# Performance work log

Measured on AMD Instinct MI355X. Metric: run time of the kernel, lower is better.

Reference implementation:

```python
import jax, jax.numpy as jnp
import numpy as np

B, L, C, H = 8, 2048, 256, 4
D = C // H  # head_dim = 64
EPS = 1e-5


def setup_inputs() -> dict:
    key = jax.random.key(0)
    ks = jax.random.split(key, 16)
    s = lambda fan_in: 1.0 / np.sqrt(fan_in)
    inp = {
        'x0': jax.random.normal(ks[0], (B, L, C), jnp.float32),
        'x1': jax.random.normal(ks[1], (B, L, C), jnp.float32),
        # attention projections (stored as (in, out); torch Linear is x @ W.T + b)
        'Wqk': jax.random.normal(ks[2], (C, C), jnp.float32) * s(C),
        'bqk': jax.random.normal(ks[3], (C,), jnp.float32) * s(C),
        'Wv': jax.random.normal(ks[4], (C, C), jnp.float32) * s(C),
        'bv': jax.random.normal(ks[5], (C,), jnp.float32) * s(C),
        'Wout': jax.random.normal(ks[6], (C, C), jnp.float32) * s(C),
        'bout': jax.random.normal(ks[7], (C,), jnp.float32) * s(C),
        # shared FFN: Linear(2C->2C) -> LayerNorm -> GELU -> Linear(2C->C)
        'W1': jax.random.normal(ks[8], (2 * C, 2 * C), jnp.float32) * s(2 * C),
        'b1': jax.random.normal(ks[9], (2 * C,), jnp.float32) * s(2 * C),
        'ln_g': jnp.ones((2 * C,), jnp.float32),
        'ln_b': jnp.zeros((2 * C,), jnp.float32),
        'W2': jax.random.normal(ks[10], (2 * C, C), jnp.float32) * s(2 * C),
        'b2': jax.random.normal(ks[11], (C,), jnp.float32) * s(2 * C),
    }
    return inp


def _heads(t):
    # (B, L, C) -> (B, H, L, D)
    b, l, _ = t.shape
    return t.reshape(b, l, H, D).transpose(0, 2, 1, 3)


def _merge(t):
    # (B, H, L, D) -> (B, L, C)
    b, h, l, d = t.shape
    return t.transpose(0, 2, 1, 3).reshape(b, l, h * d)


def _ffn(z, W1, b1, ln_g, ln_b, W2, b2):
    h = z @ W1 + b1
    mu = jnp.mean(h, axis=-1, keepdims=True)
    var = jnp.var(h, axis=-1, keepdims=True)
    h = (h - mu) * jax.lax.rsqrt(var + EPS) * ln_g + ln_b
    h = jax.nn.gelu(h, approximate=False)
    return h @ W2 + b2


def reference(x0, x1, Wqk, bqk, Wv, bv, Wout, bout, W1, b1, ln_g, ln_b, W2, b2):
    scale_sqrt = D ** (-0.25)  # sqrt(head_dim**-0.5), applied to both sides
    qk0 = _heads(x0 @ Wqk + bqk) * scale_sqrt  # (B,H,M,D)
    qk1 = _heads(x1 @ Wqk + bqk) * scale_sqrt  # (B,H,N,D)
    v0 = _heads(x0 @ Wv + bv)
    v1 = _heads(x1 @ Wv + bv)

    # single shared similarity matrix (LightGlue trick)
    sim = jnp.einsum('bhid,bhjd->bhij', qk0, qk1)  # (B,H,M,N)
    attn01 = jax.nn.softmax(sim, axis=-1)           # rows: A->B
    attn10 = jax.nn.softmax(sim, axis=-2)           # cols: B->A (softmax of sim^T along last dim)
    m0 = jnp.einsum('bhij,bhjd->bhid', attn01, v1)  # (B,H,M,D)
    m1 = jnp.einsum('bhij,bhid->bhjd', attn10, v0)  # (B,H,N,D)

    m0 = _merge(m0) @ Wout + bout
    m1 = _merge(m1) @ Wout + bout

    x0_out = x0 + _ffn(jnp.concatenate([x0, m0], axis=-1), W1, b1, ln_g, ln_b, W2, b2)
    x1_out = x1 + _ffn(jnp.concatenate([x1, m1], axis=-1), W1, b1, ln_g, ln_b, W2, b2)
    return (x0_out, x1_out)
```

## Files before the change

kernel.cpp:

```cpp
#include <hip/hip_runtime.h>
#include <hip/hip_bf16.h>

typedef _Float16 f16;
typedef _Float16 f16x8 __attribute__((ext_vector_type(8)));
typedef _Float16 f16x4 __attribute__((ext_vector_type(4)));
typedef float f32x4 __attribute__((ext_vector_type(4)));

#define MFMA16(a, b, c) __builtin_amdgcn_mfma_f32_16x16x32_f16((a), (b), (c), 0, 0, 0)
#define MFMA16K16(a, b, c) __builtin_amdgcn_mfma_f32_16x16x16f16((a), (b), (c), 0, 0, 0)

__device__ __forceinline__ void load16(const void* g, void* l) {
    __builtin_amdgcn_global_load_lds((const __attribute__((address_space(1))) void*)g,
                                     (__attribute__((address_space(3))) void*)l, 16, 0, 0);
}

__global__ __launch_bounds__(256) void k_prep(const float* __restrict__ x0,
                                              const float* __restrict__ x1,
                                              const float* __restrict__ Wqk,
                                              const float* __restrict__ Wv,
                                              const float* __restrict__ W1,
                                              const float* __restrict__ W2,
                                              const float* __restrict__ Wout,
                                              const float* __restrict__ b1,
                                              const float* __restrict__ bout,
                                              f16* __restrict__ xh, f16* __restrict__ wcat_t,
                                              f16* __restrict__ w1t, f16* __restrict__ w1bt,
                                              f16* __restrict__ w2t, f16* __restrict__ woutf16,
                                              float* __restrict__ bias_eff) {
    __shared__ float red[4];
    const int blk = blockIdx.x, tid = threadIdx.x;
    if (blk < 8192) {
        size_t i = ((size_t)blk * 256 + tid) * 4;
        const float* src = (i < 4194304) ? (x0 + i) : (x1 + (i - 4194304));
        float4 v = *(const float4*)src;
        f16x4 o = {(f16)v.x, (f16)v.y, (f16)v.z, (f16)v.w};
        *(f16x4*)(xh + i) = o;
    } else if (blk < 8704) {
        int n = blk - 8192;
        const float* W = (n < 256) ? Wqk : Wv;
        wcat_t[n * 256 + tid] = (f16)W[tid * 256 + (n & 255)];
    } else if (blk < 9216) {
        int n = blk - 8704;
        w1t[n * 512 + tid] = (f16)W1[tid * 512 + n];
    } else if (blk < 9728) {
        int n = blk - 9216;
        w1bt[n * 256 + tid] = (f16)W1[(256 + tid) * 512 + n];
    } else if (blk < 10240) {
        int j = blk - 9728;
        int n = j >> 1, k = (j & 1) * 256 + tid;
        w2t[n * 512 + k] = (f16)W2[k * 256 + n];
    } else if (blk < 10496) {
        int o = (blk - 10240) * 256 + tid;
        woutf16[o] = (f16)Wout[o];
    } else {
        int n = blk - 10496;
        float s = bout[tid] * W1[(size_t)(256 + tid) * 512 + n];
#pragma unroll
        for (int off = 1; off < 64; off <<= 1) s += __shfl_xor(s, off);
        int wave = tid >> 6, lane = tid & 63;
        if (lane == 0) red[wave] = s;
        __syncthreads();
        if (tid == 0) bias_eff[n] = b1[n] + red[0] + red[1] + red[2] + red[3];
    }
}

__global__ __launch_bounds__(256) void k_gemm(const f16* __restrict__ A1,
                                              const f16* __restrict__ A2, int ksplit,
                                              int strideA, const f16* __restrict__ Bt, int K,
                                              int N, const float* __restrict__ bias1,
                                              const float* __restrict__ bias2, int mode,
                                              void* __restrict__ out1, void* __restrict__ out2,
                                              const float* __restrict__ res1,
                                              const float* __restrict__ res2) {
    const int bn0 = blockIdx.x * 128;
    const int bm0 = blockIdx.y * 128;
    __shared__ f16 As[2][4096];
    __shared__ f16 Bs[2][4096];
    const int tid = threadIdx.x;
    const int lane = tid & 63, wave = tid >> 6;
    const int quad = lane >> 4, l16 = lane & 15;
    const int wm0 = (wave & 1) * 64, wn0 = (wave >> 1) * 64;
    const int axor = l16 & 3;

    f32x4 acc[4][4];
#pragma unroll
    for (int tm = 0; tm < 4; tm++)
#pragma unroll
        for (int tn = 0; tn < 4; tn++) acc[tm][tn] = (f32x4){0.f, 0.f, 0.f, 0.f};

    auto stage = [&](int buf, int kt) {
        const int k0 = kt * 32;
        const f16* Ab = (k0 < ksplit) ? A1 : A2;
        const int koff = (k0 < ksplit) ? k0 : k0 - ksplit;
#pragma unroll
        for (int rd = 0; rd < 2; rd++) {
            const int cbase = rd * 256 + wave * 64;
            const int c = cbase + lane;
            const int row = c >> 2, col = (c & 3) ^ (row & 3);
            load16(Ab + (size_t)(bm0 + row) * strideA + koff + col * 8, &As[buf][cbase * 8]);
        }
#pragma unroll
        for (int rd = 0; rd < 2; rd++) {
            const int cbase = rd * 256 + wave * 64;
            const int c = cbase + lane;
            const int row = c >> 2, col = (c & 3) ^ (row & 3);
            load16(Bt + (size_t)(bn0 + row) * K + k0 + col * 8, &Bs[buf][cbase * 8]);
        }
    };

    const int NT = K >> 5;
    stage(0, 0);
    __syncthreads();
    for (int kt = 0; kt < NT; kt++) {
        const int cur = kt & 1;
        if (kt + 1 < NT) stage(cur ^ 1, kt + 1);
        f16x8 af[4], bf[4];
#pragma unroll
        for (int t = 0; t < 4; t++)
            af[t] = *(const f16x8*)&As[cur][(wm0 + t * 16 + l16) * 32 + (quad ^ axor) * 8];
#pragma unroll
        for (int t = 0; t < 4; t++)
            bf[t] = *(const f16x8*)&Bs[cur][(wn0 + t * 16 + l16) * 32 + (quad ^ axor) * 8];
#pragma unroll
        for (int tm = 0; tm < 4; tm++)
#pragma unroll
            for (int tn = 0; tn < 4; tn++) acc[tm][tn] = MFMA16(bf[tn], af[tm], acc[tm][tn]);
        __syncthreads();
    }

#pragma unroll
    for (int tm = 0; tm < 4; tm++) {
        const int m = bm0 + wm0 + tm * 16 + l16;
#pragma unroll
        for (int tn = 0; tn < 4; tn++) {
            const int n = bn0 + wn0 + tn * 16 + quad * 4;
            f32x4 v = acc[tm][tn];
            if (mode == 0) {
                const int s = m >> 14, r14 = m & 16383, b = r14 >> 11, l = r14 & 2047;
                if (n < 256) {
                    float4 bi = *(const float4*)(bias1 + n);
                    const int h = n >> 6, d = n & 63;
                    const size_t hh = (size_t)((s * 8 + b) * 4 + h);
                    f16x4 o = {(f16)((v[0] + bi.x) * 0.42466090f),
                               (f16)((v[1] + bi.y) * 0.42466090f),
                               (f16)((v[2] + bi.z) * 0.42466090f),
                               (f16)((v[3] + bi.w) * 0.42466090f)};
                    *(f16x4*)((f16*)out1 + (hh * 2048 + l) * 64 + d) = o;
                } else {
                    const int n2 = n - 256;
                    float4 bi = *(const float4*)(bias2 + n2);
                    const int h = n2 >> 6, d = n2 & 63;
                    const size_t hh = (size_t)((s * 8 + b) * 4 + h);
                    f16* o2 = (f16*)out2 + (hh * 64 + d) * 2048 + l;
                    o2[0] = (f16)(v[0] + bi.x);
                    o2[2048] = (f16)(v[1] + bi.y);
                    o2[4096] = (f16)(v[2] + bi.z);
                    o2[6144] = (f16)(v[3] + bi.w);
                }
            } else if (mode == 2) {
                float4 bi = *(const float4*)(bias1 + n);
                f16x4 o = {(f16)(v[0] + bi.x), (f16)(v[1] + bi.y), (f16)(v[2] + bi.z),
                           (f16)(v[3] + bi.w)};
                *(f16x4*)((f16*)out1 + (size_t)m * N + n) = o;
            } else if (mode == 3) {
                float4 bi = *(const float4*)(bias1 + n);
                const float* xr = (m < 16384) ? (res1 + (size_t)m * 256)
                                              : (res2 + (size_t)(m - 16384) * 256);
                float4 rr = *(const float4*)(xr + n);
                float4 o = {v[0] + bi.x + rr.x, v[1] + bi.y + rr.y, v[2] + bi.z + rr.z,
                            v[3] + bi.w + rr.w};
                *(float4*)((float*)out1 + (size_t)m * 256 + n) = o;
            } else {
                f16x4 o = {(f16)v[0], (f16)v[1], (f16)v[2], (f16)v[3]};
                *(f16x4*)((f16*)out1 + (size_t)m * 512 + 256 + n) = o;
            }
        }
    }
}

__global__ __launch_bounds__(256, 4) void k_flash(const f16* __restrict__ qkbuf,
                                                  const f16* __restrict__ vtbuf,
                                                  f16* __restrict__ mbuf) {
    const int z = blockIdx.z;
    const int bh = blockIdx.y;
    const int qt = blockIdx.x;
    const size_t HSZ = 2048 * 64;
    const size_t SSZ = 32 * HSZ;
    const f16* Q = qkbuf + (z ? SSZ : 0) + bh * HSZ;
    const f16* Kp = qkbuf + (z ? 0 : SSZ) + bh * HSZ;
    const f16* Vt = vtbuf + (z ? 0 : SSZ) + bh * HSZ;
    f16* Mo = mbuf + (size_t)z * (16384 * 256);

    __shared__ f16 Ks[2][4096];
    __shared__ f16 Vs[2][4096];

    const int tid = threadIdx.x, lane = tid & 63, wave = tid >> 6;
    const int quad = lane >> 4, l16 = lane & 15;
    const int srow = lane >> 3;
    const int slc = (lane & 7) ^ (srow & 7);

    const int q0 = qt * 128 + wave * 32;
    f16x8 qf[2][2];
#pragma unroll
    for (int tq = 0; tq < 2; tq++)
#pragma unroll
        for (int kk = 0; kk < 2; kk++)
            qf[tq][kk] =
                *(const f16x8*)(Q + (size_t)(q0 + tq * 16 + l16) * 64 + kk * 32 + quad * 8);

    auto stage = [&](int buf, int kv0) {
#pragma unroll
        for (int i = 0; i < 2; i++) {
            const int widx = wave * 2 + i;
            const int row = widx * 8 + srow;
            load16(Kp + (size_t)(kv0 + row) * 64 + slc * 8, &Ks[buf][widx * 512]);
            load16(Vt + (size_t)row * 2048 + kv0 + slc * 8, &Vs[buf][widx * 512]);
        }
    };

    f32x4 oacc[4][2];
#pragma unroll
    for (int td = 0; td < 4; td++)
#pragma unroll
        for (int tq = 0; tq < 2; tq++) oacc[td][tq] = (f32x4){0.f, 0.f, 0.f, 0.f};
    float lrow[2] = {0.f, 0.f};

    stage(0, 0);
    __syncthreads();

    for (int t = 0; t < 32; t++) {
        const int cur = t & 1;
        if (t < 31) stage(cur ^ 1, (t + 1) * 64);
        const f16* Kc = Ks[cur];
        const f16* Vc = Vs[cur];

        f32x4 sacc[4][2];
#pragma unroll
        for (int tkv = 0; tkv < 4; tkv++)
#pragma unroll
            for (int tq = 0; tq < 2; tq++) sacc[tkv][tq] = (f32x4){0.f, 0.f, 0.f, 0.f};
#pragma unroll
        for (int kk = 0; kk < 2; kk++) {
#pragma unroll
            for (int tkv = 0; tkv < 4; tkv++) {
                const int r = tkv * 16 + l16;
                f16x8 ka = *(const f16x8*)(Kc + r * 64 + (((kk * 4 + quad) ^ (r & 7)) * 8));
#pragma unroll
                for (int tq = 0; tq < 2; tq++)
                    sacc[tkv][tq] = MFMA16(ka, qf[tq][kk], sacc[tkv][tq]);
            }
        }

        f16x4 pk[4][2];
#pragma unroll
        for (int tq = 0; tq < 2; tq++) {
            float rs = 0.f;
#pragma unroll
            for (int tkv = 0; tkv < 4; tkv++) {
                float p0 = __builtin_amdgcn_exp2f(sacc[tkv][tq][0] - 8.0f);
                float p1 = __builtin_amdgcn_exp2f(sacc[tkv][tq][1] - 8.0f);
                float p2 = __builtin_amdgcn_exp2f(sacc[tkv][tq][2] - 8.0f);
                float p3 = __builtin_amdgcn_exp2f(sacc[tkv][tq][3] - 8.0f);
                pk[tkv][tq] = (f16x4){(f16)p0, (f16)p1, (f16)p2, (f16)p3};
                rs += (p0 + p1) + (p2 + p3);
            }
            lrow[tq] += rs;
        }

#pragma unroll
        for (int tkv = 0; tkv < 4; tkv++) {
#pragma unroll
            for (int td = 0; td < 4; td++) {
                const int r = td * 16 + l16;
                f16x4 va = *(const f16x4*)(Vc + r * 64 +
                                           (((2 * tkv + (quad >> 1)) ^ (r & 7)) * 8) +
                                           (quad & 1) * 4);
#pragma unroll
                for (int tq = 0; tq < 2; tq++)
                    oacc[td][tq] = MFMA16K16(va, pk[tkv][tq], oacc[td][tq]);
            }
        }
        __syncthreads();
    }

    const int b = bh >> 2, h = bh & 3;
#pragma unroll
    for (int tq = 0; tq < 2; tq++) {
        float ls = lrow[tq];
        ls += __shfl_xor(ls, 16);
        ls += __shfl_xor(ls, 32);
        const float inv = 1.f / ls;
        const int q = q0 + tq * 16 + l16;
        const size_t base = ((size_t)(b * 2048 + q)) * 256 + h * 64;
#pragma unroll
        for (int td = 0; td < 4; td++) {
            f16x4 o = {(f16)(oacc[td][tq][0] * inv), (f16)(oacc[td][tq][1] * inv),
                       (f16)(oacc[td][tq][2] * inv), (f16)(oacc[td][tq][3] * inv)};
            *(f16x4*)(Mo + base + td * 16 + quad * 4) = o;
        }
    }
}

__global__ __launch_bounds__(256) void k_ln_gelu(f16* __restrict__ h,
                                                 const float* __restrict__ g,
                                                 const float* __restrict__ bb) {
    const int tid = threadIdx.x, wave = tid >> 6, lane = tid & 63;
    const size_t row = (size_t)blockIdx.x * 4 + wave;
    f16* hr = h + row * 512 + lane * 8;
    f16x8 v = *(const f16x8*)hr;
    float x[8];
    float s = 0.f, sq = 0.f;
#pragma unroll
    for (int i = 0; i < 8; i++) {
        x[i] = (float)v[i];
        s += x[i];
        sq += x[i] * x[i];
    }
#pragma unroll
    for (int off = 1; off < 64; off <<= 1) {
        s += __shfl_xor(s, off);
        sq += __shfl_xor(sq, off);
    }
    const float mu = s * (1.f / 512.f);
    const float var = sq * (1.f / 512.f) - mu * mu;
    const float rstd = rsqrtf(var + 1e-5f);
    float4 g0 = *(const float4*)(g + lane * 8), g1 = *(const float4*)(g + lane * 8 + 4);
    float4 b0 = *(const float4*)(bb + lane * 8), b1 = *(const float4*)(bb + lane * 8 + 4);
    float gg[8] = {g0.x, g0.y, g0.z, g0.w, g1.x, g1.y, g1.z, g1.w};
    float bv[8] = {b0.x, b0.y, b0.z, b0.w, b1.x, b1.y, b1.z, b1.w};
#pragma unroll
    for (int i = 0; i < 8; i++) {
        float a = (x[i] - mu) * rstd * gg[i] + bv[i];
        a = 0.5f * a * (1.f + erff(a * 0.70710678118f));
        v[i] = (f16)a;
    }
    *(f16x8*)hr = v;
}


extern "C" void kernel_launch(void* const* d_in, const int* in_sizes, int n_in, void* d_out,
                              int out_size, void* d_ws, size_t ws_size, hipStream_t stream) {
    const float* x0 = (const float*)d_in[0];
    const float* x1 = (const float*)d_in[1];
    const float* Wqk = (const float*)d_in[2];
    const float* bqk = (const float*)d_in[3];
    const float* Wv = (const float*)d_in[4];
    const float* bv = (const float*)d_in[5];
    const float* Wout = (const float*)d_in[6];
    const float* bout = (const float*)d_in[7];
    const float* W1 = (const float*)d_in[8];
    const float* b1 = (const float*)d_in[9];
    const float* lng = (const float*)d_in[10];
    const float* lnb = (const float*)d_in[11];
    const float* W2 = (const float*)d_in[12];
    const float* b2 = (const float*)d_in[13];
    float* out = (float*)d_out;

    char* ws = (char*)d_ws;
    f16* xh = (f16*)(ws);
    f16* qk = (f16*)(ws + 16777216);
    f16* vt = (f16*)(ws + 33554432);
    f16* mbuf = (f16*)(ws + 50331648);
    f16* hbuf = qk;
    f16* w1bt = (f16*)(ws + 16777216);
    f16* woutf16 = w1bt + 131072;
    f16* wcat_t = (f16*)(ws + 67108864);
    f16* w1t = wcat_t + 131072;
    f16* w2t = w1t + 262144;
    float* bias_eff = (float*)(w2t + 131072);

    k_prep<<<11008, 256, 0, stream>>>(x0, x1, Wqk, Wv, W1, W2, Wout, b1, bout, xh, wcat_t, w1t,
                                      w1bt, w2t, woutf16, bias_eff);
    k_gemm<<<dim3(2, 4), 256, 0, stream>>>(w1bt, w1bt, 1 << 30, 256, woutf16, 256, 256, nullptr,
                                           nullptr, 4, w1t, nullptr, nullptr, nullptr);
    k_gemm<<<dim3(4, 256), 256, 0, stream>>>(xh, xh, 1 << 30, 256, wcat_t, 256, 512, bqk, bv, 0,
                                             qk, vt, nullptr, nullptr);
    k_flash<<<dim3(16, 32, 2), 256, 0, stream>>>(qk, vt, mbuf);
    k_gemm<<<dim3(4, 256), 256, 0, stream>>>(xh, mbuf, 256, 256, w1t, 512, 512, bias_eff,
                                             nullptr, 2, hbuf, nullptr, nullptr, nullptr);
    k_ln_gelu<<<8192, 256, 0, stream>>>(hbuf, lng, lnb);
    k_gemm<<<dim3(2, 256), 256, 0, stream>>>(hbuf, hbuf, 1 << 30, 512, w2t, 512, 256, b2, nullptr,
                                             3, out, nullptr, x0, x1);
}
```

Measured before the change: 327.3 us.

## Fuse LayerNorm+GELU into FFN1 GEMM and fold Wout product into prep

Adds a dedicated FFN1 GEMM kernel where each block computes full 512-wide rows (64 rows per block), so the LayerNorm statistics and GELU can be applied in the epilogue. This removes the separate ln_gelu pass and its round trip of the hidden buffer through memory. It also computes the folded Wout·W1b weight inside the prep kernel with scalar FMAs, replacing a tiny extra GEMM launch. In the flash kernel the -8 softmax offset moves into the score accumulator's initial value, which saves one subtract per exp. The trade-offs are a large per-block tile (4x8 MFMA accumulators per wave, 64 KB B buffers) that limits occupancy, and only 512 blocks in the FFN1 grid.

Measured after the change: 365.0 us. +11.5%, slower.

```diff
diff --git a/kernel.cpp b/kernel.cpp
--- a/kernel.cpp
+++ b/kernel.cpp
@@ -24,9 +24,9 @@
                                               const float* __restrict__ b1,
                                               const float* __restrict__ bout,
                                               f16* __restrict__ xh, f16* __restrict__ wcat_t,
-                                              f16* __restrict__ w1t, f16* __restrict__ w1bt,
-                                              f16* __restrict__ w2t, f16* __restrict__ woutf16,
+                                              f16* __restrict__ w1t, f16* __restrict__ w2t,
                                               float* __restrict__ bias_eff) {
+    __shared__ float lbuf[256];
     __shared__ float red[4];
     const int blk = blockIdx.x, tid = threadIdx.x;
     if (blk < 8192) {
@@ -43,17 +43,20 @@
         int n = blk - 8704;
         w1t[n * 512 + tid] = (f16)W1[tid * 512 + n];
     } else if (blk < 9728) {
-        int n = blk - 9216;
-        w1bt[n * 256 + tid] = (f16)W1[(256 + tid) * 512 + n];
-    } else if (blk < 10240) {
-        int j = blk - 9728;
+        int j = blk - 9216;
         int n = j >> 1, k = (j & 1) * 256 + tid;
         w2t[n * 512 + k] = (f16)W2[k * 256 + n];
-    } else if (blk < 10496) {
-        int o = (blk - 10240) * 256 + tid;
-        woutf16[o] = (f16)Wout[o];
+    } else if (blk < 10240) {
+        int n = blk - 9728;
+        lbuf[tid] = W1[(size_t)(256 + tid) * 512 + n];
+        __syncthreads();
+        const float* wr = Wout + (size_t)tid * 256;
+        float s = 0.f;
+#pragma unroll 8
+        for (int t = 0; t < 256; t++) s += lbuf[t] * wr[t];
+        w1t[n * 512 + 256 + tid] = (f16)s;
     } else {
-        int n = blk - 10496;
+        int n = blk - 10240;
         float s = bout[tid] * W1[(size_t)(256 + tid) * 512 + n];
 #pragma unroll
         for (int off = 1; off < 64; off <<= 1) s += __shfl_xor(s, off);
@@ -157,12 +160,7 @@
                     o2[4096] = (f16)(v[2] + bi.z);
                     o2[6144] = (f16)(v[3] + bi.w);
                 }
-            } else if (mode == 2) {
-                float4 bi = *(const float4*)(bias1 + n);
-                f16x4 o = {(f16)(v[0] + bi.x), (f16)(v[1] + bi.y), (f16)(v[2] + bi.z),
-                           (f16)(v[3] + bi.w)};
-                *(f16x4*)((f16*)out1 + (size_t)m * N + n) = o;
-            } else if (mode == 3) {
+            } else {
                 float4 bi = *(const float4*)(bias1 + n);
                 const float* xr = (m < 16384) ? (res1 + (size_t)m * 256)
                                               : (res2 + (size_t)(m - 16384) * 256);
@@ -170,10 +168,125 @@
                 float4 o = {v[0] + bi.x + rr.x, v[1] + bi.y + rr.y, v[2] + bi.z + rr.z,
                             v[3] + bi.w + rr.w};
                 *(float4*)((float*)out1 + (size_t)m * 256 + n) = o;
-            } else {
-                f16x4 o = {(f16)v[0], (f16)v[1], (f16)v[2], (f16)v[3]};
-                *(f16x4*)((f16*)out1 + (size_t)m * 512 + 256 + n) = o;
-            }
+            }
+        }
+    }
+}
+
+__global__ __launch_bounds__(256, 2) void k_ffn1(const f16* __restrict__ A1,
+                                                 const f16* __restrict__ A2,
+                                                 const f16* __restrict__ Bt,
+                                                 const float* __restrict__ bias,
+                                                 const float* __restrict__ g,
+                                                 const float* __restrict__ bb,
+                                                 f16* __restrict__ out) {
+    const int bm0 = blockIdx.x * 64;
+    __shared__ f16 As[2][2048];
+    __shared__ f16 Bs[2][16384];
+    __shared__ float redS[4][64], redQ[4][64];
+    const int tid = threadIdx.x;
+    const int lane = tid & 63, wave = tid >> 6;
+    const int quad = lane >> 4, l16 = lane & 15;
+    const int wn0 = wave * 128;
+    const int axor = l16 & 3;
+
+    f32x4 acc[4][8];
+#pragma unroll
+    for (int tm = 0; tm < 4; tm++)
+#pragma unroll
+        for (int tn = 0; tn < 8; tn++) acc[tm][tn] = (f32x4){0.f, 0.f, 0.f, 0.f};
+
+    auto stage = [&](int buf, int kt) {
+        const int k0 = kt * 32;
+        const f16* Ab = (k0 < 256) ? A1 : A2;
+        const int koff = (k0 < 256) ? k0 : k0 - 256;
+        {
+            const int row = tid >> 2, col = (tid & 3) ^ (row & 3);
+            load16(Ab + (size_t)(bm0 + row) * 256 + koff + col * 8, &As[buf][(tid & ~63) * 8]);
+        }
+#pragma unroll
+        for (int i = 0; i < 8; i++) {
+            const int cbase = i * 256 + (tid & ~63);
+            const int c = cbase + (tid & 63);
+            const int row = c >> 2, col = (c & 3) ^ (row & 3);
+            load16(Bt + (size_t)row * 512 + k0 + col * 8, &Bs[buf][cbase * 8]);
+        }
+    };
+
+    stage(0, 0);
+    __syncthreads();
+    for (int kt = 0; kt < 16; kt++) {
+        const int cur = kt & 1;
+        if (kt + 1 < 16) stage(cur ^ 1, kt + 1);
+        f16x8 af[4], bf[8];
+#pragma unroll
+        for (int t = 0; t < 4; t++)
+            af[t] = *(const f16x8*)&As[cur][(t * 16 + l16) * 32 + (quad ^ axor) * 8];
+#pragma unroll
+        for (int t = 0; t < 8; t++)
+            bf[t] = *(const f16x8*)&Bs[cur][(wn0 + t * 16 + l16) * 32 + (quad ^ axor) * 8];
+#pragma unroll
+        for (int tm = 0; tm < 4; tm++)
+#pragma unroll
+            for (int tn = 0; tn < 8; tn++) acc[tm][tn] = MFMA16(bf[tn], af[tm], acc[tm][tn]);
+        __syncthreads();
+    }
+
+    float s[4], q[4];
+#pragma unroll
+    for (int tm = 0; tm < 4; tm++) {
+        s[tm] = 0.f;
+        q[tm] = 0.f;
+#pragma unroll
+        for (int tn = 0; tn < 8; tn++) {
+            const int n = wn0 + tn * 16 + quad * 4;
+            float4 bi = *(const float4*)(bias + n);
+            acc[tm][tn][0] += bi.x;
+            acc[tm][tn][1] += bi.y;
+            acc[tm][tn][2] += bi.z;
+            acc[tm][tn][3] += bi.w;
+#pragma unroll
+            for (int r = 0; r < 4; r++) {
+                s[tm] += acc[tm][tn][r];
+                q[tm] += acc[tm][tn][r] * acc[tm][tn][r];
+            }
+        }
+        s[tm] += __shfl_xor(s[tm], 16);
+        s[tm] += __shfl_xor(s[tm], 32);
+        q[tm] += __shfl_xor(q[tm], 16);
+        q[tm] += __shfl_xor(q[tm], 32);
+    }
+    if (quad == 0) {
+#pragma unroll
+        for (int tm = 0; tm < 4; tm++) {
+            redS[wave][tm * 16 + l16] = s[tm];
+            redQ[wave][tm * 16 + l16] = q[tm];
+        }
+    }
+    __syncthreads();
+#pragma unroll
+    for (int tm = 0; tm < 4; tm++) {
+        const int mr = tm * 16 + l16;
+        const float st = redS[0][mr] + redS[1][mr] + redS[2][mr] + redS[3][mr];
+        const float qt = redQ[0][mr] + redQ[1][mr] + redQ[2][mr] + redQ[3][mr];
+        const float mu = st * (1.f / 512.f);
+        const float var = qt * (1.f / 512.f) - mu * mu;
+        const float rstd = rsqrtf(var + 1e-5f);
+        const size_t m = bm0 + mr;
+#pragma unroll
+        for (int tn = 0; tn < 8; tn++) {
+            const int n = wn0 + tn * 16 + quad * 4;
+            float4 gg = *(const float4*)(g + n);
+            float4 bv = *(const float4*)(bb + n);
+            f16x4 o;
+#pragma unroll
+            for (int r = 0; r < 4; r++) {
+                float a = (acc[tm][tn][r] - mu) * rstd * ((const float*)&gg)[r] +
+                          ((const float*)&bv)[r];
+                a = 0.5f * a * (1.f + erff(a * 0.70710678118f));
+                o[r] = (f16)a;
+            }
+            *(f16x4*)(out + m * 512 + n) = o;
         }
     }
 }
@@ -238,7 +351,8 @@
 #pragma unroll
         for (int tkv = 0; tkv < 4; tkv++)
 #pragma unroll
-            for (int tq = 0; tq < 2; tq++) sacc[tkv][tq] = (f32x4){0.f, 0.f, 0.f, 0.f};
+            for (int tq = 0; tq < 2; tq++)
+                sacc[tkv][tq] = (f32x4){-8.f, -8.f, -8.f, -8.f};
 #pragma unroll
         for (int kk = 0; kk < 2; kk++) {
 #pragma unroll
@@ -257,10 +371,10 @@
             float rs = 0.f;
 #pragma unroll
             for (int tkv = 0; tkv < 4; tkv++) {
-                float p0 = __builtin_amdgcn_exp2f(sacc[tkv][tq][0] - 8.0f);
-                float p1 = __builtin_amdgcn_exp2f(sacc[tkv][tq][1] - 8.0f);
-                float p2 = __builtin_amdgcn_exp2f(sacc[tkv][tq][2] - 8.0f);
-                float p3 = __builtin_amdgcn_exp2f(sacc[tkv][tq][3] - 8.0f);
+                float p0 = __builtin_amdgcn_exp2f(sacc[tkv][tq][0]);
+                float p1 = __builtin_amdgcn_exp2f(sacc[tkv][tq][1]);
+                float p2 = __builtin_amdgcn_exp2f(sacc[tkv][tq][2]);
+                float p3 = __builtin_amdgcn_exp2f(sacc[tkv][tq][3]);
                 pk[tkv][tq] = (f16x4){(f16)p0, (f16)p1, (f16)p2, (f16)p3};
                 rs += (p0 + p1) + (p2 + p3);
             }
@@ -299,42 +413,6 @@
             *(f16x4*)(Mo + base + td * 16 + quad * 4) = o;
         }
     }
-}
-
-__global__ __launch_bounds__(256) void k_ln_gelu(f16* __restrict__ h,
-                                                 const float* __restrict__ g,
-                                                 const float* __restrict__ bb) {
-    const int tid = threadIdx.x, wave = tid >> 6, lane = tid & 63;
-    const size_t row = (size_t)blockIdx.x * 4 + wave;
-    f16* hr = h + row * 512 + lane * 8;
-    f16x8 v = *(const f16x8*)hr;
-    float x[8];
-    float s = 0.f, sq = 0.f;
-#pragma unroll
-    for (int i = 0; i < 8; i++) {
-        x[i] = (float)v[i];
-        s += x[i];
-        sq += x[i] * x[i];
-    }
-#pragma unroll
-    for (int off = 1; off < 64; off <<= 1) {
-        s += __shfl_xor(s, off);
-        sq += __shfl_xor(sq, off);
-    }
-    const float mu = s * (1.f / 512.f);
-    const float var = sq * (1.f / 512.f) - mu * mu;
-    const float rstd = rsqrtf(var + 1e-5f);
-    float4 g0 = *(const float4*)(g + lane * 8), g1 = *(const float4*)(g + lane * 8 + 4);
-    float4 b0 = *(const float4*)(bb + lane * 8), b1 = *(const float4*)(bb + lane * 8 + 4);
-    float gg[8] = {g0.x, g0.y, g0.z, g0.w, g1.x, g1.y, g1.z, g1.w};
-    float bv[8] = {b0.x, b0.y, b0.z, b0.w, b1.x, b1.y, b1.z, b1.w};
-#pragma unroll
-    for (int i = 0; i < 8; i++) {
-        float a = (x[i] - mu) * rstd * gg[i] + bv[i];
-        a = 0.5f * a * (1.f + erff(a * 0.70710678118f));
-        v[i] = (f16)a;
-    }
-    *(f16x8*)hr = v;
 }
 
 
@@ -362,23 +440,17 @@
     f16* vt = (f16*)(ws + 33554432);
     f16* mbuf = (f16*)(ws + 50331648);
     f16* hbuf = qk;
-    f16* w1bt = (f16*)(ws + 16777216);
-    f16* woutf16 = w1bt + 131072;
     f16* wcat_t = (f16*)(ws + 67108864);
     f16* w1t = wcat_t + 131072;
     f16* w2t = w1t + 262144;
     float* bias_eff = (float*)(w2t + 131072);
 
-    k_prep<<<11008, 256, 0, stream>>>(x0, x1, Wqk, Wv, W1, W2, Wout, b1, bout, xh, wcat_t, w1t,
-                                      w1bt, w2t, woutf16, bias_eff);
-    k_gemm<<<dim3(2, 4), 256, 0, stream>>>(w1bt, w1bt, 1 << 30, 256, woutf16, 256, 256, nullptr,
-                                           nullptr, 4, w1t, nullptr, nullptr, nullptr);
+    k_prep<<<10752, 256, 0, stream>>>(x0, x1, Wqk, Wv, W1, W2, Wout, b1, bout, xh, wcat_t, w1t,
+                                      w2t, bias_eff);
     k_gemm<<<dim3(4, 256), 256, 0, stream>>>(xh, xh, 1 << 30, 256, wcat_t, 256, 512, bqk, bv, 0,
                                              qk, vt, nullptr, nullptr);
     k_flash<<<dim3(16, 32, 2), 256, 0, stream>>>(qk, vt, mbuf);
-    k_gemm<<<dim3(4, 256), 256, 0, stream>>>(xh, mbuf, 256, 256, w1t, 512, 512, bias_eff,
-                                             nullptr, 2, hbuf, nullptr, nullptr, nullptr);
-    k_ln_gelu<<<8192, 256, 0, stream>>>(hbuf, lng, lnb);
+    k_ffn1<<<512, 256, 0, stream>>>(xh, mbuf, w1t, bias_eff, lng, lnb, hbuf);
     k_gemm<<<dim3(2, 256), 256, 0, stream>>>(hbuf, hbuf, 1 << 30, 512, w2t, 512, 256, b2, nullptr,
                                              3, out, nullptr, x0, x1);
 }
```

## Halve flash-attention query tile per wave and swap grid axes for locality

Applied to the files above, without the earlier changes.

Each wave now handles 16 query rows instead of 32, so a block covers 64 queries and the grid doubles to 2048 blocks. Block indexing is swapped so consecutive blocks share a query tile across heads, and launch bounds are raised to 5 blocks per SIMD to allow more occupancy. The aim is more parallelism and lower register pressure. In exchange, each K/V tile staged in LDS is reused by half as many MFMAs, so total K/V traffic through LDS and L2 doubles.

Measured after the change: 334.8 us. 1.02x slower.

```diff
diff --git a/kernel.cpp b/kernel.cpp
--- a/kernel.cpp
+++ b/kernel.cpp
@@ -178,12 +178,12 @@
     }
 }
 
-__global__ __launch_bounds__(256, 4) void k_flash(const f16* __restrict__ qkbuf,
+__global__ __launch_bounds__(256, 5) void k_flash(const f16* __restrict__ qkbuf,
                                                   const f16* __restrict__ vtbuf,
                                                   f16* __restrict__ mbuf) {
     const int z = blockIdx.z;
-    const int bh = blockIdx.y;
-    const int qt = blockIdx.x;
+    const int bh = blockIdx.x;
+    const int qt = blockIdx.y;
     const size_t HSZ = 2048 * 64;
     const size_t SSZ = 32 * HSZ;
     const f16* Q = qkbuf + (z ? SSZ : 0) + bh * HSZ;
@@ -199,14 +199,11 @@
     const int srow = lane >> 3;
     const int slc = (lane & 7) ^ (srow & 7);
 
-    const int q0 = qt * 128 + wave * 32;
-    f16x8 qf[2][2];
-#pragma unroll
-    for (int tq = 0; tq < 2; tq++)
-#pragma unroll
-        for (int kk = 0; kk < 2; kk++)
-            qf[tq][kk] =
-                *(const f16x8*)(Q + (size_t)(q0 + tq * 16 + l16) * 64 + kk * 32 + quad * 8);
+    const int q0 = qt * 64 + wave * 16;
+    f16x8 qf[2];
+#pragma unroll
+    for (int kk = 0; kk < 2; kk++)
+        qf[kk] = *(const f16x8*)(Q + (size_t)(q0 + l16) * 64 + kk * 32 + quad * 8);
 
     auto stage = [&](int buf, int kv0) {
 #pragma unroll
@@ -218,12 +215,10 @@
         }
     };
 
-    f32x4 oacc[4][2];
-#pragma unroll
-    for (int td = 0; td < 4; td++)
-#pragma unroll
-        for (int tq = 0; tq < 2; tq++) oacc[td][tq] = (f32x4){0.f, 0.f, 0.f, 0.f};
-    float lrow[2] = {0.f, 0.f};
+    f32x4 oacc[4];
+#pragma unroll
+    for (int td = 0; td < 4; td++) oacc[td] = (f32x4){0.f, 0.f, 0.f, 0.f};
+    float lrow = 0.f;
 
     stage(0, 0);
     __syncthreads();
@@ -234,37 +229,32 @@
         const f16* Kc = Ks[cur];
         const f16* Vc = Vs[cur];
 
-        f32x4 sacc[4][2];
-#pragma unroll
-        for (int tkv = 0; tkv < 4; tkv++)
-#pragma unroll
-            for (int tq = 0; tq < 2; tq++) sacc[tkv][tq] = (f32x4){0.f, 0.f, 0.f, 0.f};
+        f32x4 sacc[4];
+#pragma unroll
+        for (int tkv = 0; tkv < 4; tkv++) sacc[tkv] = (f32x4){0.f, 0.f, 0.f, 0.f};
 #pragma unroll
         for (int kk = 0; kk < 2; kk++) {
 #pragma unroll
             for (int tkv = 0; tkv < 4; tkv++) {
                 const int r = tkv * 16 + l16;
                 f16x8 ka = *(const f16x8*)(Kc + r * 64 + (((kk * 4 + quad) ^ (r & 7)) * 8));
-#pragma unroll
-                for (int tq = 0; tq < 2; tq++)
-                    sacc[tkv][tq] = MFMA16(ka, qf[tq][kk], sacc[tkv][tq]);
+                sacc[tkv] = MFMA16(ka, qf[kk], sacc[tkv]);
             }
         }
 
-        f16x4 pk[4][2];
-#pragma unroll
-        for (int tq = 0; tq < 2; tq++) {
+        f16x4 pk[4];
+        {
             float rs = 0.f;
 #pragma unroll
             for (int tkv = 0; tkv < 4; tkv++) {
-                float p0 = __builtin_amdgcn_exp2f(sacc[tkv][tq][0] - 8.0f);
-                float p1 = __builtin_amdgcn_exp2f(sacc[tkv][tq][1] - 8.0f);
-                float p2 = __builtin_amdgcn_exp2f(sacc[tkv][tq][2] - 8.0f);
-                float p3 = __builtin_amdgcn_exp2f(sacc[tkv][tq][3] - 8.0f);
-                pk[tkv][tq] = (f16x4){(f16)p0, (f16)p1, (f16)p2, (f16)p3};
+                float p0 = __builtin_amdgcn_exp2f(sacc[tkv][0] - 8.0f);
+                float p1 = __builtin_amdgcn_exp2f(sacc[tkv][1] - 8.0f);
+                float p2 = __builtin_amdgcn_exp2f(sacc[tkv][2] - 8.0f);
+                float p3 = __builtin_amdgcn_exp2f(sacc[tkv][3] - 8.0f);
+                pk[tkv] = (f16x4){(f16)p0, (f16)p1, (f16)p2, (f16)p3};
                 rs += (p0 + p1) + (p2 + p3);
             }
-            lrow[tq] += rs;
+            lrow += rs;
         }
 
 #pragma unroll
@@ -275,29 +265,24 @@
                 f16x4 va = *(const f16x4*)(Vc + r * 64 +
                                            (((2 * tkv + (quad >> 1)) ^ (r & 7)) * 8) +
                                            (quad & 1) * 4);
-#pragma unroll
-                for (int tq = 0; tq < 2; tq++)
-                    oacc[td][tq] = MFMA16K16(va, pk[tkv][tq], oacc[td][tq]);
+                oacc[td] = MFMA16K16(va, pk[tkv], oacc[td]);
             }
         }
         __syncthreads();
     }
 
     const int b = bh >> 2, h = bh & 3;
-#pragma unroll
-    for (int tq = 0; tq < 2; tq++) {
-        float ls = lrow[tq];
-        ls += __shfl_xor(ls, 16);
-        ls += __shfl_xor(ls, 32);
-        const float inv = 1.f / ls;
-        const int q = q0 + tq * 16 + l16;
-        const size_t base = ((size_t)(b * 2048 + q)) * 256 + h * 64;
-#pragma unroll
-        for (int td = 0; td < 4; td++) {
-            f16x4 o = {(f16)(oacc[td][tq][0] * inv), (f16)(oacc[td][tq][1] * inv),
-                       (f16)(oacc[td][tq][2] * inv), (f16)(oacc[td][tq][3] * inv)};
-            *(f16x4*)(Mo + base + td * 16 + quad * 4) = o;
-        }
+    float ls = lrow;
+    ls += __shfl_xor(ls, 16);
+    ls += __shfl_xor(ls, 32);
+    const float inv = 1.f / ls;
+    const int q = q0 + l16;
+    const size_t base = ((size_t)(b * 2048 + q)) * 256 + h * 64;
+#pragma unroll
+    for (int td = 0; td < 4; td++) {
+        f16x4 o = {(f16)(oacc[td][0] * inv), (f16)(oacc[td][1] * inv),
+                   (f16)(oacc[td][2] * inv), (f16)(oacc[td][3] * inv)};
+        *(f16x4*)(Mo + base + td * 16 + quad * 4) = o;
     }
 }
 
@@ -375,7 +360,7 @@
                                            nullptr, 4, w1t, nullptr, nullptr, nullptr);
     k_gemm<<<dim3(4, 256), 256, 0, stream>>>(xh, xh, 1 << 30, 256, wcat_t, 256, 512, bqk, bv, 0,
                                              qk, vt, nullptr, nullptr);
-    k_flash<<<dim3(16, 32, 2), 256, 0, stream>>>(qk, vt, mbuf);
+    k_flash<<<dim3(32, 32, 2), 256, 0, stream>>>(qk, vt, mbuf);
     k_gemm<<<dim3(4, 256), 256, 0, stream>>>(xh, mbuf, 256, 256, w1t, 512, 512, bias_eff,
                                              nullptr, 2, hbuf, nullptr, nullptr, nullptr);
     k_ln_gelu<<<8192, 256, 0, stream>>>(hbuf, lng, lnb);
```

## Widen GEMM tiles to 128x256, swap grid order, read fp16 residual

Applied to the files above, without the earlier changes.

The GEMM kernel now computes a 128x256 output tile per block, with each wave owning 64x128 and holding 32 accumulators. This is meant to raise A-tile reuse and cut the number of blocks. Grid axes are swapped so M blocks vary fastest, likewise for the flash kernel (head fastest), which changes L2 locality. The final GEMM reads the residual from the fp16 copy of x instead of fp32 x0/x1, which saves bandwidth but adds fp16 rounding to the residual. The larger register footprint (launch_bounds 256,2) may lower occupancy.

New measurement: 318.2 us. 1.03x faster.

```diff
diff --git a/kernel.cpp b/kernel.cpp
--- a/kernel.cpp
+++ b/kernel.cpp
@@ -64,29 +64,28 @@
     }
 }
 
-__global__ __launch_bounds__(256) void k_gemm(const f16* __restrict__ A1,
-                                              const f16* __restrict__ A2, int ksplit,
-                                              int strideA, const f16* __restrict__ Bt, int K,
-                                              int N, const float* __restrict__ bias1,
-                                              const float* __restrict__ bias2, int mode,
-                                              void* __restrict__ out1, void* __restrict__ out2,
-                                              const float* __restrict__ res1,
-                                              const float* __restrict__ res2) {
-    const int bn0 = blockIdx.x * 128;
-    const int bm0 = blockIdx.y * 128;
+__global__ __launch_bounds__(256, 2) void k_gemm(const f16* __restrict__ A1,
+                                                 const f16* __restrict__ A2, int ksplit,
+                                                 int strideA, const f16* __restrict__ Bt, int K,
+                                                 int N, const float* __restrict__ bias1,
+                                                 const float* __restrict__ bias2, int mode,
+                                                 void* __restrict__ out1, void* __restrict__ out2,
+                                                 const f16* __restrict__ resh) {
+    const int bm0 = blockIdx.x * 128;
+    const int bn0 = blockIdx.y * 256;
     __shared__ f16 As[2][4096];
-    __shared__ f16 Bs[2][4096];
+    __shared__ f16 Bs[2][8192];
     const int tid = threadIdx.x;
     const int lane = tid & 63, wave = tid >> 6;
     const int quad = lane >> 4, l16 = lane & 15;
-    const int wm0 = (wave & 1) * 64, wn0 = (wave >> 1) * 64;
+    const int wm0 = (wave & 1) * 64, wn0 = (wave >> 1) * 128;
     const int axor = l16 & 3;
 
-    f32x4 acc[4][4];
+    f32x4 acc[4][8];
 #pragma unroll
     for (int tm = 0; tm < 4; tm++)
 #pragma unroll
-        for (int tn = 0; tn < 4; tn++) acc[tm][tn] = (f32x4){0.f, 0.f, 0.f, 0.f};
+        for (int tn = 0; tn < 8; tn++) acc[tm][tn] = (f32x4){0.f, 0.f, 0.f, 0.f};
 
     auto stage = [&](int buf, int kt) {
         const int k0 = kt * 32;
@@ -100,7 +99,7 @@
             load16(Ab + (size_t)(bm0 + row) * strideA + koff + col * 8, &As[buf][cbase * 8]);
         }
 #pragma unroll
-        for (int rd = 0; rd < 2; rd++) {
+        for (int rd = 0; rd < 4; rd++) {
             const int cbase = rd * 256 + wave * 64;
             const int c = cbase + lane;
             const int row = c >> 2, col = (c & 3) ^ (row & 3);
@@ -114,17 +113,17 @@
     for (int kt = 0; kt < NT; kt++) {
         const int cur = kt & 1;
         if (kt + 1 < NT) stage(cur ^ 1, kt + 1);
-        f16x8 af[4], bf[4];
+        f16x8 af[4], bf[8];
 #pragma unroll
         for (int t = 0; t < 4; t++)
             af[t] = *(const f16x8*)&As[cur][(wm0 + t * 16 + l16) * 32 + (quad ^ axor) * 8];
 #pragma unroll
-        for (int t = 0; t < 4; t++)
+        for (int t = 0; t < 8; t++)
             bf[t] = *(const f16x8*)&Bs[cur][(wn0 + t * 16 + l16) * 32 + (quad ^ axor) * 8];
 #pragma unroll
         for (int tm = 0; tm < 4; tm++)
 #pragma unroll
-            for (int tn = 0; tn < 4; tn++) acc[tm][tn] = MFMA16(bf[tn], af[tm], acc[tm][tn]);
+            for (int tn = 0; tn < 8; tn++) acc[tm][tn] = MFMA16(bf[tn], af[tm], acc[tm][tn]);
         __syncthreads();
     }
 
@@ -132,7 +131,7 @@
     for (int tm = 0; tm < 4; tm++) {
         const int m = bm0 + wm0 + tm * 16 + l16;
 #pragma unroll
-        for (int tn = 0; tn < 4; tn++) {
+        for (int tn = 0; tn < 8; tn++) {
             const int n = bn0 + wn0 + tn * 16 + quad * 4;
             f32x4 v = acc[tm][tn];
             if (mode == 0) {
@@ -164,11 +163,9 @@
                 *(f16x4*)((f16*)out1 + (size_t)m * N + n) = o;
             } else if (mode == 3) {
                 float4 bi = *(const float4*)(bias1 + n);
-                const float* xr = (m < 16384) ? (res1 + (size_t)m * 256)
-                                              : (res2 + (size_t)(m - 16384) * 256);
-                float4 rr = *(const float4*)(xr + n);
-                float4 o = {v[0] + bi.x + rr.x, v[1] + bi.y + rr.y, v[2] + bi.z + rr.z,
-                            v[3] + bi.w + rr.w};
+                f16x4 rr = *(const f16x4*)(resh + (size_t)m * 256 + n);
+                float4 o = {v[0] + bi.x + (float)rr[0], v[1] + bi.y + (float)rr[1],
+                            v[2] + bi.z + (float)rr[2], v[3] + bi.w + (float)rr[3]};
                 *(float4*)((float*)out1 + (size_t)m * 256 + n) = o;
             } else {
                 f16x4 o = {(f16)v[0], (f16)v[1], (f16)v[2], (f16)v[3]};
@@ -182,8 +179,8 @@
                                                   const f16* __restrict__ vtbuf,
                                                   f16* __restrict__ mbuf) {
     const int z = blockIdx.z;
-    const int bh = blockIdx.y;
-    const int qt = blockIdx.x;
+    const int bh = blockIdx.x;
+    const int qt = blockIdx.y;
     const size_t HSZ = 2048 * 64;
     const size_t SSZ = 32 * HSZ;
     const f16* Q = qkbuf + (z ? SSZ : 0) + bh * HSZ;
@@ -371,14 +368,14 @@
 
     k_prep<<<11008, 256, 0, stream>>>(x0, x1, Wqk, Wv, W1, W2, Wout, b1, bout, xh, wcat_t, w1t,
                                       w1bt, w2t, woutf16, bias_eff);
-    k_gemm<<<dim3(2, 4), 256, 0, stream>>>(w1bt, w1bt, 1 << 30, 256, woutf16, 256, 256, nullptr,
-                                           nullptr, 4, w1t, nullptr, nullptr, nullptr);
-    k_gemm<<<dim3(4, 256), 256, 0, stream>>>(xh, xh, 1 << 30, 256, wcat_t, 256, 512, bqk, bv, 0,
-                                             qk, vt, nullptr, nullptr);
-    k_flash<<<dim3(16, 32, 2), 256, 0, stream>>>(qk, vt, mbuf);
-    k_gemm<<<dim3(4, 256), 256, 0, stream>>>(xh, mbuf, 256, 256, w1t, 512, 512, bias_eff,
-                                             nullptr, 2, hbuf, nullptr, nullptr, nullptr);
+    k_gemm<<<dim3(4, 1), 256, 0, stream>>>(w1bt, w1bt, 1 << 30, 256, woutf16, 256, 256, nullptr,
+                                           nullptr, 4, w1t, nullptr, nullptr);
+    k_gemm<<<dim3(256, 2), 256, 0, stream>>>(xh, xh, 1 << 30, 256, wcat_t, 256, 512, bqk, bv, 0,
+                                             qk, vt, nullptr);
+    k_flash<<<dim3(32, 16, 2), 256, 0, stream>>>(qk, vt, mbuf);
+    k_gemm<<<dim3(256, 2), 256, 0, stream>>>(xh, mbuf, 256, 256, w1t, 512, 512, bias_eff,
+                                             nullptr, 2, hbuf, nullptr, nullptr);
     k_ln_gelu<<<8192, 256, 0, stream>>>(hbuf, lng, lnb);
-    k_gemm<<<dim3(2, 256), 256, 0, stream>>>(hbuf, hbuf, 1 << 30, 512, w2t, 512, 256, b2, nullptr,
-                                             3, out, nullptr, x0, x1);
-}
+    k_gemm<<<dim3(256, 1), 256, 0, stream>>>(hbuf, hbuf, 1 << 30, 512, w2t, 512, 256, b2,
+                                             nullptr, 3, out, nullptr, xh);
+}
```
